# Performance work log

Measured on AMD Instinct MI355X. Metric: run time of the kernel, lower is better.

Reference implementation:

```python
import jax, jax.numpy as jnp
import numpy as np
import math

NUM_USER, NUM_COURSE, NUM_TEACHER, NUM_SCHOOL = 100000, 10000, 5000, 3000
D = 16
B, LS, LT, LSC = 1024, 200, 10, 5
NC, LU, LS2, LT2 = 100, 50, 3, 5


def setup_inputs() -> dict:
    key = jax.random.key(0)
    ks = jax.random.split(key, 32)
    sig = 1.0 / D  # torch init: normal(0, 1/num_dim) on ALL params (overwrites padding row too)
    p = lambda k, shp: jax.random.normal(k, shp, jnp.float32) * sig
    ri = lambda k, shp, hi: jax.random.randint(k, shp, 0, hi)
    inp = {}
    inp['user_idx']       = ri(ks[0], (B, 1), NUM_USER)
    inp['user_sequence']  = ri(ks[1], (B, LS), NUM_COURSE + 1)   # may hit padding idx
    inp['user_teachers']  = ri(ks[2], (B, LT), NUM_TEACHER + 1)
    inp['user_school']    = ri(ks[3], (B, LSC), NUM_SCHOOL + 1)
    inp['user_len_seq']     = jax.random.randint(ks[4], (B, 1), 1, LS + 1).astype(jnp.float32)
    inp['user_len_teacher'] = jax.random.randint(ks[5], (B, 1), 1, LT + 1).astype(jnp.float32)
    inp['user_len_school']  = jax.random.randint(ks[6], (B, 1), 1, LSC + 1).astype(jnp.float32)
    inp['course_set']     = ri(ks[7], (B, NC), NUM_COURSE)
    inp['course_user']    = ri(ks[8], (B, NC, LU), NUM_USER + 1)
    inp['course_school']  = ri(ks[9], (B, NC, LS2), NUM_SCHOOL + 1)
    inp['course_teacher'] = ri(ks[10], (B, NC, LT2), NUM_TEACHER + 1)
    inp['course_len_u']       = jax.random.randint(ks[11], (B, NC), 1, LU + 1).astype(jnp.float32)
    inp['course_len_teacher'] = jax.random.randint(ks[12], (B, NC), 1, LT2 + 1).astype(jnp.float32)
    # learned parameters (jax layout: Linear weight is [in, out])
    inp['user_table']    = p(ks[13], (NUM_USER + 1, D))
    inp['course_table']  = p(ks[14], (NUM_COURSE + 1, D))
    inp['teacher_table'] = p(ks[15], (NUM_TEACHER + 1, D))
    inp['school_table']  = p(ks[16], (NUM_SCHOOL + 1, D))
    inp['Qw'] = p(ks[17], (D, D)); inp['Qb'] = p(ks[18], (D,))
    inp['Kw'] = p(ks[19], (D, D)); inp['Kb'] = p(ks[20], (D,))
    inp['g1w'] = p(ks[21], (2 * D, D)); inp['g1b'] = p(ks[22], (D,))
    inp['g2w'] = p(ks[23], (D, D));     inp['g2b'] = p(ks[24], (D,))
    inp['caw1'] = p(ks[25], (D, D)); inp['cab1'] = p(ks[26], (D,))
    inp['caw2'] = p(ks[27], (D, 1))
    return inp


def _transformer(x, Qw, Qb, Kw, Kb):
    # x: [B, L, d] -> [B, d]. Faithful to source: K is RESHAPED (not transposed) to [B, d, L].
    b, L, d = x.shape
    Q = jax.nn.relu(x @ Qw + Qb)                       # [B, L, d]
    K = jax.nn.relu(x @ Kw + Kb).reshape(b, d, L)      # reshape, as in source
    s = jnp.matmul(Q, K) / math.sqrt(d)                # [B, L, L]
    s = jnp.where(jnp.eye(L, dtype=bool), jnp.float32(1e-32), s)  # diag set to 1e-32
    su = jax.nn.softmax(s, axis=2)
    a = jnp.matmul(su, x)                              # [B, L, d]
    return a.mean(axis=1)


def reference(user_idx, user_sequence, user_teachers, user_school,
              user_len_seq, user_len_teacher, user_len_school,
              course_set, course_user, course_school, course_teacher,
              course_len_u, course_len_teacher,
              user_table, course_table, teacher_table, school_table,
              Qw, Qb, Kw, Kb, g1w, g1b, g2w, g2b, caw1, cab1, caw2):
    # ---- user side ----
    user_emb = user_table[user_idx[:, 0]]                       # [B, d]
    seq_emb = course_table[user_sequence]                       # [B, LS, d]
    seq_rep = _transformer(seq_emb, Qw, Qb, Kw, Kb)             # [B, d]
    ut_mean = teacher_table[user_teachers].sum(axis=1) / user_len_teacher
    us_mean = school_table[user_school].sum(axis=1) / user_len_school
    agg = (seq_rep + ut_mean + us_mean) / 3.0
    h = jnp.concatenate([user_emb, agg], axis=1)                # [B, 2d]
    user_final = jax.nn.relu(h @ g1w + g1b) @ g2w + g2b         # [B, d]
    # ---- course side ----
    course_emb = course_table[course_set]                       # [B, Nc, d]
    cu_mean = user_table[course_user].sum(axis=2) / course_len_u[..., None]
    cs_sum  = school_table[course_school].sum(axis=2)           # note: no division (as in source)
    ct_mean = teacher_table[course_teacher].sum(axis=2) / course_len_teacher[..., None]
    nb = jnp.stack([cu_mean, cs_sum, ct_mean], axis=2)          # [B, Nc, 3, d]
    att = jax.nn.softmax(jax.nn.sigmoid(nb @ caw1 + cab1) @ caw2, axis=2)
    _course_agg = (nb * att).sum(axis=2)  # computed in source but unused (dead code)
    # ---- score ----
    out = jnp.sum(user_final[:, None, :] * course_emb, axis=2)  # [B, Nc]
    return out
```

## Files before the change

### kernel.cpp

```cpp
#include <hip/hip_runtime.h>
#include <hip/hip_bf16.h>

#define NBATCH 1024
#define LSEQ   200
#define DD     16
#define LTT    10
#define LSCH   5
#define NCC    100

#define XT_S   232
#define KT_S   24

#define QSCALE 0.3606737602f

typedef __bf16 bf16_4 __attribute__((ext_vector_type(4)));
typedef float  f32x4  __attribute__((ext_vector_type(4)));
typedef short  short4v __attribute__((ext_vector_type(4)));
typedef unsigned int uint2v __attribute__((ext_vector_type(2)));

__device__ __forceinline__ int kswz(int j) { return ((j >> 3) ^ (j >> 6)) & 1; }

__device__ __forceinline__ f32x4 mfma16(bf16_4 a, bf16_4 b, f32x4 c) {
#if __has_builtin(__builtin_amdgcn_mfma_f32_16x16x16bf16_1k)
    return __builtin_amdgcn_mfma_f32_16x16x16bf16_1k(
        __builtin_bit_cast(short4v, a), __builtin_bit_cast(short4v, b), c, 0, 0, 0);
#else
    uint2v au = __builtin_bit_cast(uint2v, a);
    uint2v bu = __builtin_bit_cast(uint2v, b);
    asm("v_mfma_f32_16x16x16_bf16 %0, %1, %2, %0" : "+v"(c) : "v"(au), "v"(bu));
    return c;
#endif
}

__global__ __launch_bounds__(256, 4) void hin_kernel(
    const int*   __restrict__ user_idx,
    const int*   __restrict__ user_sequence,
    const int*   __restrict__ user_teachers,
    const int*   __restrict__ user_school,
    const float* __restrict__ user_len_teacher,
    const float* __restrict__ user_len_school,
    const int*   __restrict__ course_set,
    const float* __restrict__ user_table,
    const float* __restrict__ course_table,
    const float* __restrict__ teacher_table,
    const float* __restrict__ school_table,
    const float* __restrict__ Qw, const float* __restrict__ Qb,
    const float* __restrict__ Kw, const float* __restrict__ Kb,
    const float* __restrict__ g1w, const float* __restrict__ g1b,
    const float* __restrict__ g2w, const float* __restrict__ g2b,
    float*       __restrict__ out)
{
    __shared__ __align__(16) __bf16 xt[DD * XT_S];
    __shared__ __align__(16) __bf16 kt[208 * KT_S];
    __shared__ float red[4][DD];
    __shared__ __align__(16) float tot12t[64];
    __shared__ float uf[DD];
    __shared__ float gst[800];
    __shared__ float rows_pre[256];
    __shared__ float lens[2];

    const int b    = blockIdx.x;
    const int t    = threadIdx.x;
    const int w    = t >> 6;
    const int lane = t & 63;
    const int grp  = lane >> 4;
    const int li   = lane & 15;

    if (t < 128)
        xt[(t >> 3)*XT_S + 200 + (t & 7)] = (__bf16)0.f;
    else {
        const int i = t - 128;
        kt[(200 + (i >> 4))*KT_S + (i & 15)] = (__bf16)0.f;
    }
    for (int i = t; i < 800; i += 256) {
        float v;
        if      (i < 512) v = g1w[i];
        else if (i < 528) v = g1b[i - 512];
        else if (i < 784) v = g2w[i - 528];
        else              v = g2b[i - 784];
        gst[i] = v;
    }
    if (t < 16)       rows_pre[t] = user_table[user_idx[b]*DD + t];
    else if (t < 176) { const int i = t - 16;
        rows_pre[t] = teacher_table[user_teachers[b*LTT + (i >> 4)]*DD + (i & 15)]; }
    else if (t < 256) { const int i = t - 176;
        rows_pre[t] = school_table[user_school[b*LSCH + (i >> 4)]*DD + (i & 15)]; }
    if (t == 0) { lens[0] = user_len_teacher[b]; lens[1] = user_len_school[b]; }

    const int wu = __builtin_amdgcn_readfirstlane(w);
    const int dr = li - grp*4;

    bf16_4 qf0, qf1, qf2, qf12;
    {
        bf16_4 wq, wk;
        #pragma unroll
        for (int e = 0; e < 4; e++) {
            wq[e] = (__bf16)(Qw[(grp*4 + e)*DD + li] * QSCALE);
            wk[e] = (__bf16)(Kw[(grp*4 + e)*DD + li]);
        }
        const float4 qb4 = *(const float4*)&Qb[grp*4];
        float qbias[4] = {qb4.x*QSCALE, qb4.y*QSCALE, qb4.z*QSCALE, qb4.w*QSCALE};
        const float kbias = Kb[li];

        auto compute_qk = [&](int l0, bf16_4& qout, bool do_scatter) {
            const int lrow = l0 + li;
            const int idx = (lrow < LSEQ) ? user_sequence[b*LSEQ + lrow] : 0;
            const float4 xv = *(const float4*)&course_table[idx*DD + grp*4];
            bf16_4 xf;
            xf[0] = (__bf16)xv.x; xf[1] = (__bf16)xv.y;
            xf[2] = (__bf16)xv.z; xf[3] = (__bf16)xv.w;
            if (do_scatter && lrow < LSEQ) {
                #pragma unroll
                for (int e = 0; e < 4; e++)
                    xt[(grp*4 + e)*XT_S + lrow] = xf[e];
            }
            const f32x4 zc = {0.f, 0.f, 0.f, 0.f};
            f32x4 qv = mfma16(wq, xf, zc);
            f32x4 kv = mfma16(xf, wk, zc);
            #pragma unroll
            for (int r = 0; r < 4; r++)
                qout[r] = (__bf16)fmaxf(qv[r] + qbias[r], 0.f);
            if (do_scatter) {
                #pragma unroll
                for (int r = 0; r < 4; r++) {
                    const int krow = l0 + grp*4 + r;
                    if (krow < LSEQ) {
                        const float val = fmaxf(kv[r] + kbias, 0.f);
                        const int f = krow*DD + li;
                        const int p = f / 200;
                        const int j = f - p*200;
                        kt[j*KT_S + (p ^ (kswz(j) << 3))] = (__bf16)val;
                    }
                }
            }
        };
        compute_qk(wu*16,       qf0, true);
        compute_qk((wu+4)*16,   qf1, true);
        compute_qk((wu+8)*16,   qf2, true);
        compute_qk(192,         qf12, wu == 0);
    }
    __syncthreads();

    bf16_4 onesb;
    #pragma unroll
    for (int i = 0; i < 4; i++) onesb[i] = (__bf16)1.0f;

    const int mt0 = wu, mt1 = wu + 4, mt2 = wu + 8;
    const int jlo = (wu == 0) ? 0 : (3*wu + 1);
    const int jhi = 3*wu + 4;

    f32x4 ao0 = {0.f,0.f,0.f,0.f}, aD0 = {0.f,0.f,0.f,0.f};
    f32x4 ao1 = {0.f,0.f,0.f,0.f}, aD1 = {0.f,0.f,0.f,0.f};
    f32x4 ao2 = {0.f,0.f,0.f,0.f}, aD2 = {0.f,0.f,0.f,0.f};
    f32x4 ao3 = {0.f,0.f,0.f,0.f}, aD3 = {0.f,0.f,0.f,0.f};

    #pragma unroll
    for (int jt = 0; jt < 13; jt++) {
        const int jr = jt*16 + li;
        const bf16_4 kf = *(const bf16_4*)&kt[jr*KT_S + ((grp*4) ^ (kswz(jr) << 3))];
        const bf16_4 xb = *(const bf16_4*)&xt[li*XT_S + jt*16 + grp*4];
        const f32x4 zc = {0.f, 0.f, 0.f, 0.f};
        f32x4 s0 = mfma16(kf, qf0, zc);
        f32x4 s1 = mfma16(kf, qf1, zc);
        f32x4 s2 = mfma16(kf, qf2, zc);
        bf16_4 p0, p1, p2;
        #pragma unroll
        for (int r = 0; r < 4; r++) {
            float v0 = __builtin_amdgcn_exp2f(s0[r]);
            float v1 = __builtin_amdgcn_exp2f(s1[r]);
            float v2 = __builtin_amdgcn_exp2f(s2[r]);
            if (jt == 12 && grp >= 2) { v0 = 0.f; v1 = 0.f; v2 = 0.f; }
            if (jt == mt0 && dr == r) v0 = 1.0f;
            if (jt == mt1 && dr == r) v1 = 1.0f;
            if (jt == mt2 && dr == r) v2 = 1.0f;
            p0[r] = (__bf16)v0; p1[r] = (__bf16)v1; p2[r] = (__bf16)v2;
        }
        aD0 = mfma16(p0, onesb, aD0);  ao0 = mfma16(p0, xb, ao0);
        aD1 = mfma16(p1, onesb, aD1);  ao1 = mfma16(p1, xb, ao1);
        aD2 = mfma16(p2, onesb, aD2);  ao2 = mfma16(p2, xb, ao2);
        if (jt >= jlo && jt < jhi) {
            f32x4 s3 = mfma16(kf, qf12, zc);
            bf16_4 p3;
            #pragma unroll
            for (int r = 0; r < 4; r++) {
                float v3 = __builtin_amdgcn_exp2f(s3[r]);
                if (jt == 12 && grp >= 2) v3 = 0.f;
                if (jt == 12 && dr == r)  v3 = 1.0f;
                p3[r] = (__bf16)v3;
            }
            aD3 = mfma16(p3, onesb, aD3);  ao3 = mfma16(p3, xb, ao3);
        }
    }

    float wsum = 0.f;
    #pragma unroll
    for (int r = 0; r < 4; r++) {
        wsum += ao0[r] * __builtin_amdgcn_rcpf(aD0[r]);
        wsum += ao1[r] * __builtin_amdgcn_rcpf(aD1[r]);
        wsum += ao2[r] * __builtin_amdgcn_rcpf(aD2[r]);
    }
    if (li == 0) {
        #pragma unroll
        for (int r = 0; r < 4; r++)
            tot12t[(grp*4 + r)*4 + w] = aD3[r];
    }
    __syncthreads();

    #pragma unroll
    for (int r = 0; r < 4; r++) {
        const int q = grp*4 + r;
        const float4 p4 = *(const float4*)&tot12t[q*4];
        const float dsum = (p4.x + p4.y) + (p4.z + p4.w);
        if (192 + q < LSEQ)
            wsum += ao3[r] * __builtin_amdgcn_rcpf(dsum);
    }

    wsum += __shfl_xor(wsum, 16);
    wsum += __shfl_xor(wsum, 32);
    if (lane < DD) red[w][lane] = wsum;
    __syncthreads();

    float4 ce0, ce1, ce2, ce3;
    if (t < NCC) {
        const int ci = course_set[b*NCC + t];
        const float* ce = &course_table[ci*DD];
        ce0 = *(const float4*)&ce[0];
        ce1 = *(const float4*)&ce[4];
        ce2 = *(const float4*)&ce[8];
        ce3 = *(const float4*)&ce[12];
    }

    if (w == 0) {
        const float ue  = rows_pre[li];
        const float seq = (red[0][li] + red[1][li] + red[2][li] + red[3][li]) * (1.0f / LSEQ);
        float uts = 0.f;
        #pragma unroll
        for (int i = 0; i < LTT; i++)  uts += rows_pre[16 + i*16 + li];
        float uss = 0.f;
        #pragma unroll
        for (int i = 0; i < LSCH; i++) uss += rows_pre[176 + i*16 + li];
        const float agg = (seq + uts / lens[0] + uss / lens[1]) * (1.0f / 3.0f);
        float a1 = gst[512 + li];
        #pragma unroll
        for (int k = 0; k < 16; k++) a1 = fmaf(__shfl(ue,  k), gst[k*DD + li], a1);
        #pragma unroll
        for (int k = 0; k < 16; k++) a1 = fmaf(__shfl(agg, k), gst[(16 + k)*DD + li], a1);
        const float hidv = fmaxf(a1, 0.f);
        float a2 = gst[784 + li];
        #pragma unroll
        for (int k = 0; k < 16; k++) a2 = fmaf(__shfl(hidv, k), gst[528 + k*DD + li], a2);
        if (lane < DD) uf[lane] = a2;
    }
    __syncthreads();

    if (t < NCC) {
        const float4 u0 = *(const float4*)&uf[0];
        const float4 u1 = *(const float4*)&uf[4];
        const float4 u2 = *(const float4*)&uf[8];
        const float4 u3 = *(const float4*)&uf[12];
        float s = ce0.x*u0.x + ce0.y*u0.y + ce0.z*u0.z + ce0.w*u0.w;
        s      += ce1.x*u1.x + ce1.y*u1.y + ce1.z*u1.z + ce1.w*u1.w;
        s      += ce2.x*u2.x + ce2.y*u2.y + ce2.z*u2.z + ce2.w*u2.w;
        s      += ce3.x*u3.x + ce3.y*u3.y + ce3.z*u3.z + ce3.w*u3.w;
        out[b*NCC + t] = s;
    }
}

extern "C" void kernel_launch(void* const* d_in, const int* in_sizes, int n_in,
                              void* d_out, int out_size, void* d_ws, size_t ws_size,
                              hipStream_t stream) {
    const int*   user_idx         = (const int*)  d_in[0];
    const int*   user_sequence    = (const int*)  d_in[1];
    const int*   user_teachers    = (const int*)  d_in[2];
    const int*   user_school      = (const int*)  d_in[3];
    const float* user_len_teacher = (const float*)d_in[5];
    const float* user_len_school  = (const float*)d_in[6];
    const int*   course_set       = (const int*)  d_in[7];
    const float* user_table       = (const float*)d_in[13];
    const float* course_table     = (const float*)d_in[14];
    const float* teacher_table    = (const float*)d_in[15];
    const float* school_table     = (const float*)d_in[16];
    const float* Qw  = (const float*)d_in[17];
    const float* Qb  = (const float*)d_in[18];
    const float* Kw  = (const float*)d_in[19];
    const float* Kb  = (const float*)d_in[20];
    const float* g1w = (const float*)d_in[21];
    const float* g1b = (const float*)d_in[22];
    const float* g2w = (const float*)d_in[23];
    const float* g2b = (const float*)d_in[24];

    float* outp = (float*)d_out;

    hipLaunchKernelGGL(hin_kernel, dim3(NBATCH), dim3(256), 0, stream,
                       user_idx, user_sequence, user_teachers, user_school,
                       user_len_teacher, user_len_school, course_set,
                       user_table, course_table, teacher_table, school_table,
                       Qw, Qb, Kw, Kb, g1w, g1b, g2w, g2b, outp);
}
```

Measured before the change: 20.24 us.

## Split attention across two blocks per batch and move the MLP tail into a second kernel

The single fused kernel becomes two kernels. The attention kernel launches two blocks per batch row, each handling half of the query tiles with at most two tiles per wave, and writes its partial sums to workspace. A small tail kernel then gathers the user, teacher and school embeddings, runs the MLP and computes the course scores. The aim is more parallelism and occupancy (launch bounds raised to 8) with lower register pressure. In exchange, both blocks recompute the full Q/K projection and LDS staging, and the split adds a second launch plus a global-memory round trip.

```diff
diff --git a/kernel.cpp b/kernel.cpp
--- a/kernel.cpp
+++ b/kernel.cpp
@@ -32,34 +32,20 @@
 #endif
 }
 
-__global__ __launch_bounds__(256, 4) void hin_kernel(
-    const int*   __restrict__ user_idx,
+__global__ __launch_bounds__(256, 8) void hin_attn(
     const int*   __restrict__ user_sequence,
-    const int*   __restrict__ user_teachers,
-    const int*   __restrict__ user_school,
-    const float* __restrict__ user_len_teacher,
-    const float* __restrict__ user_len_school,
-    const int*   __restrict__ course_set,
-    const float* __restrict__ user_table,
     const float* __restrict__ course_table,
-    const float* __restrict__ teacher_table,
-    const float* __restrict__ school_table,
     const float* __restrict__ Qw, const float* __restrict__ Qb,
     const float* __restrict__ Kw, const float* __restrict__ Kb,
-    const float* __restrict__ g1w, const float* __restrict__ g1b,
-    const float* __restrict__ g2w, const float* __restrict__ g2b,
-    float*       __restrict__ out)
+    float*       __restrict__ ws)
 {
     __shared__ __align__(16) __bf16 xt[DD * XT_S];
     __shared__ __align__(16) __bf16 kt[208 * KT_S];
     __shared__ float red[4][DD];
-    __shared__ __align__(16) float tot12t[64];
-    __shared__ float uf[DD];
-    __shared__ float gst[800];
-    __shared__ float rows_pre[256];
-    __shared__ float lens[2];
-
-    const int b    = blockIdx.x;
+
+    const int bid  = blockIdx.x;
+    const int b    = bid >> 1;
+    const int q    = bid & 1;
     const int t    = threadIdx.x;
     const int w    = t >> 6;
     const int lane = t & 63;
@@ -72,20 +58,6 @@
         const int i = t - 128;
         kt[(200 + (i >> 4))*KT_S + (i & 15)] = (__bf16)0.f;
     }
-    for (int i = t; i < 800; i += 256) {
-        float v;
-        if      (i < 512) v = g1w[i];
-        else if (i < 528) v = g1b[i - 512];
-        else if (i < 784) v = g2w[i - 528];
-        else              v = g2b[i - 784];
-        gst[i] = v;
-    }
-    if (t < 16)       rows_pre[t] = user_table[user_idx[b]*DD + t];
-    else if (t < 176) { const int i = t - 16;
-        rows_pre[t] = teacher_table[user_teachers[b*LTT + (i >> 4)]*DD + (i & 15)]; }
-    else if (t < 256) { const int i = t - 176;
-        rows_pre[t] = school_table[user_school[b*LSCH + (i >> 4)]*DD + (i & 15)]; }
-    if (t == 0) { lens[0] = user_len_teacher[b]; lens[1] = user_len_school[b]; }
 
     const int wu = __builtin_amdgcn_readfirstlane(w);
     const int dr = li - grp*4;
@@ -134,91 +106,83 @@
                 }
             }
         };
-        compute_qk(wu*16,       qf0, true);
-        compute_qk((wu+4)*16,   qf1, true);
-        compute_qk((wu+8)*16,   qf2, true);
-        compute_qk(192,         qf12, wu == 0);
+        compute_qk(wu*16,     qf0, true);
+        compute_qk((wu+4)*16, qf1, true);
+        compute_qk((wu+8)*16, qf2, true);
+        compute_qk(192,       qf12, wu == 0);
     }
     __syncthreads();
+
+    int tA, tB; bool hasB; bf16_4 qfA, qfB;
+    if (q == 0)       { tA = wu;     qfA = qf0; tB = wu + 4; qfB = qf1;  hasB = (wu != 3); }
+    else if (wu == 0) { tA = 8;      qfA = qf2; tB = 12;     qfB = qf12; hasB = true; }
+    else if (wu == 3) { tA = 7;      qfA = qf1; tB = 11;     qfB = qf2;  hasB = true; }
+    else              { tA = 8 + wu; qfA = qf2; tB = 0;      qfB = qf0;  hasB = false; }
 
     bf16_4 onesb;
     #pragma unroll
     for (int i = 0; i < 4; i++) onesb[i] = (__bf16)1.0f;
 
-    const int mt0 = wu, mt1 = wu + 4, mt2 = wu + 8;
-    const int jlo = (wu == 0) ? 0 : (3*wu + 1);
-    const int jhi = 3*wu + 4;
-
-    f32x4 ao0 = {0.f,0.f,0.f,0.f}, aD0 = {0.f,0.f,0.f,0.f};
-    f32x4 ao1 = {0.f,0.f,0.f,0.f}, aD1 = {0.f,0.f,0.f,0.f};
-    f32x4 ao2 = {0.f,0.f,0.f,0.f}, aD2 = {0.f,0.f,0.f,0.f};
-    f32x4 ao3 = {0.f,0.f,0.f,0.f}, aD3 = {0.f,0.f,0.f,0.f};
-
-    #pragma unroll
-    for (int jt = 0; jt < 13; jt++) {
-        const int jr = jt*16 + li;
-        const bf16_4 kf = *(const bf16_4*)&kt[jr*KT_S + ((grp*4) ^ (kswz(jr) << 3))];
-        const bf16_4 xb = *(const bf16_4*)&xt[li*XT_S + jt*16 + grp*4];
-        const f32x4 zc = {0.f, 0.f, 0.f, 0.f};
-        f32x4 s0 = mfma16(kf, qf0, zc);
-        f32x4 s1 = mfma16(kf, qf1, zc);
-        f32x4 s2 = mfma16(kf, qf2, zc);
-        bf16_4 p0, p1, p2;
-        #pragma unroll
-        for (int r = 0; r < 4; r++) {
-            float v0 = __builtin_amdgcn_exp2f(s0[r]);
-            float v1 = __builtin_amdgcn_exp2f(s1[r]);
-            float v2 = __builtin_amdgcn_exp2f(s2[r]);
-            if (jt == 12 && grp >= 2) { v0 = 0.f; v1 = 0.f; v2 = 0.f; }
-            if (jt == mt0 && dr == r) v0 = 1.0f;
-            if (jt == mt1 && dr == r) v1 = 1.0f;
-            if (jt == mt2 && dr == r) v2 = 1.0f;
-            p0[r] = (__bf16)v0; p1[r] = (__bf16)v1; p2[r] = (__bf16)v2;
-        }
-        aD0 = mfma16(p0, onesb, aD0);  ao0 = mfma16(p0, xb, ao0);
-        aD1 = mfma16(p1, onesb, aD1);  ao1 = mfma16(p1, xb, ao1);
-        aD2 = mfma16(p2, onesb, aD2);  ao2 = mfma16(p2, xb, ao2);
-        if (jt >= jlo && jt < jhi) {
-            f32x4 s3 = mfma16(kf, qf12, zc);
-            bf16_4 p3;
+    float wsum = 0.f;
+    auto attend = [&](int mt, bf16_4 qf) {
+        f32x4 ao = {0.f,0.f,0.f,0.f}, aD = {0.f,0.f,0.f,0.f};
+        #pragma unroll
+        for (int jt = 0; jt < 13; jt++) {
+            const int jr = jt*16 + li;
+            const bf16_4 kf = *(const bf16_4*)&kt[jr*KT_S + ((grp*4) ^ (kswz(jr) << 3))];
+            const bf16_4 xb = *(const bf16_4*)&xt[li*XT_S + jt*16 + grp*4];
+            const f32x4 zc = {0.f, 0.f, 0.f, 0.f};
+            f32x4 s = mfma16(kf, qf, zc);
+            bf16_4 p;
             #pragma unroll
             for (int r = 0; r < 4; r++) {
-                float v3 = __builtin_amdgcn_exp2f(s3[r]);
-                if (jt == 12 && grp >= 2) v3 = 0.f;
-                if (jt == 12 && dr == r)  v3 = 1.0f;
-                p3[r] = (__bf16)v3;
+                float v = __builtin_amdgcn_exp2f(s[r]);
+                if (jt == 12 && grp >= 2) v = 0.f;
+                if (jt == mt && dr == r)  v = 1.0f;
+                p[r] = (__bf16)v;
             }
-            aD3 = mfma16(p3, onesb, aD3);  ao3 = mfma16(p3, xb, ao3);
+            aD = mfma16(p, onesb, aD);
+            ao = mfma16(p, xb, ao);
         }
-    }
-
-    float wsum = 0.f;
-    #pragma unroll
-    for (int r = 0; r < 4; r++) {
-        wsum += ao0[r] * __builtin_amdgcn_rcpf(aD0[r]);
-        wsum += ao1[r] * __builtin_amdgcn_rcpf(aD1[r]);
-        wsum += ao2[r] * __builtin_amdgcn_rcpf(aD2[r]);
-    }
-    if (li == 0) {
-        #pragma unroll
-        for (int r = 0; r < 4; r++)
-            tot12t[(grp*4 + r)*4 + w] = aD3[r];
-    }
-    __syncthreads();
-
-    #pragma unroll
-    for (int r = 0; r < 4; r++) {
-        const int q = grp*4 + r;
-        const float4 p4 = *(const float4*)&tot12t[q*4];
-        const float dsum = (p4.x + p4.y) + (p4.z + p4.w);
-        if (192 + q < LSEQ)
-            wsum += ao3[r] * __builtin_amdgcn_rcpf(dsum);
-    }
+        #pragma unroll
+        for (int r = 0; r < 4; r++) {
+            const int grow = mt*16 + grp*4 + r;
+            if (grow < LSEQ)
+                wsum += ao[r] * __builtin_amdgcn_rcpf(aD[r]);
+        }
+    };
+    attend(tA, qfA);
+    if (hasB) attend(tB, qfB);
 
     wsum += __shfl_xor(wsum, 16);
     wsum += __shfl_xor(wsum, 32);
     if (lane < DD) red[w][lane] = wsum;
     __syncthreads();
+
+    if (t < DD)
+        ws[(b*2 + q)*DD + t] = (red[0][t] + red[1][t]) + (red[2][t] + red[3][t]);
+}
+
+__global__ __launch_bounds__(128) void hin_tail(
+    const int*   __restrict__ user_idx,
+    const int*   __restrict__ user_teachers,
+    const int*   __restrict__ user_school,
+    const float* __restrict__ user_len_teacher,
+    const float* __restrict__ user_len_school,
+    const int*   __restrict__ course_set,
+    const float* __restrict__ user_table,
+    const float* __restrict__ course_table,
+    const float* __restrict__ teacher_table,
+    const float* __restrict__ school_table,
+    const float* __restrict__ g1w, const float* __restrict__ g1b,
+    const float* __restrict__ g2w, const float* __restrict__ g2b,
+    const float* __restrict__ ws,
+    float*       __restrict__ out)
+{
+    __shared__ float uf[DD];
+
+    const int b = blockIdx.x;
+    const int t = threadIdx.x;
 
     float4 ce0, ce1, ce2, ce3;
     if (t < NCC) {
@@ -230,26 +194,29 @@
         ce3 = *(const float4*)&ce[12];
     }
 
-    if (w == 0) {
-        const float ue  = rows_pre[li];
-        const float seq = (red[0][li] + red[1][li] + red[2][li] + red[3][li]) * (1.0f / LSEQ);
+    if (t < 64) {
+        const int li = t & 15;
+        const float seq = (ws[b*2*DD + li] + ws[(b*2 + 1)*DD + li]) * (1.0f / LSEQ);
+        const float ue  = user_table[user_idx[b]*DD + li];
         float uts = 0.f;
         #pragma unroll
-        for (int i = 0; i < LTT; i++)  uts += rows_pre[16 + i*16 + li];
+        for (int i = 0; i < LTT; i++)
+            uts += teacher_table[user_teachers[b*LTT + i]*DD + li];
         float uss = 0.f;
         #pragma unroll
-        for (int i = 0; i < LSCH; i++) uss += rows_pre[176 + i*16 + li];
-        const float agg = (seq + uts / lens[0] + uss / lens[1]) * (1.0f / 3.0f);
-        float a1 = gst[512 + li];
-        #pragma unroll
-        for (int k = 0; k < 16; k++) a1 = fmaf(__shfl(ue,  k), gst[k*DD + li], a1);
-        #pragma unroll
-        for (int k = 0; k < 16; k++) a1 = fmaf(__shfl(agg, k), gst[(16 + k)*DD + li], a1);
+        for (int i = 0; i < LSCH; i++)
+            uss += school_table[user_school[b*LSCH + i]*DD + li];
+        const float agg = (seq + uts / user_len_teacher[b] + uss / user_len_school[b]) * (1.0f / 3.0f);
+        float a1 = g1b[li];
+        #pragma unroll
+        for (int k = 0; k < 16; k++) a1 = fmaf(__shfl(ue,  k), g1w[k*DD + li], a1);
+        #pragma unroll
+        for (int k = 0; k < 16; k++) a1 = fmaf(__shfl(agg, k), g1w[(16 + k)*DD + li], a1);
         const float hidv = fmaxf(a1, 0.f);
-        float a2 = gst[784 + li];
-        #pragma unroll
-        for (int k = 0; k < 16; k++) a2 = fmaf(__shfl(hidv, k), gst[528 + k*DD + li], a2);
-        if (lane < DD) uf[lane] = a2;
+        float a2 = g2b[li];
+        #pragma unroll
+        for (int k = 0; k < 16; k++) a2 = fmaf(__shfl(hidv, k), g2w[k*DD + li], a2);
+        if (t < DD) uf[t] = a2;
     }
     __syncthreads();
 
@@ -290,10 +257,13 @@
     const float* g2b = (const float*)d_in[24];
 
     float* outp = (float*)d_out;
-
-    hipLaunchKernelGGL(hin_kernel, dim3(NBATCH), dim3(256), 0, stream,
-                       user_idx, user_sequence, user_teachers, user_school,
+    float* ws   = (float*)d_ws;
+
+    hipLaunchKernelGGL(hin_attn, dim3(NBATCH*2), dim3(256), 0, stream,
+                       user_sequence, course_table, Qw, Qb, Kw, Kb, ws);
+    hipLaunchKernelGGL(hin_tail, dim3(NBATCH), dim3(128), 0, stream,
+                       user_idx, user_teachers, user_school,
                        user_len_teacher, user_len_school, course_set,
                        user_table, course_table, teacher_table, school_table,
-                       Qw, Qb, Kw, Kb, g1w, g1b, g2w, g2b, outp);
-}
+                       g1w, g1b, g2w, g2b, ws, outp);
+}
```

Result: slower. 28.96 us (+43.1%).

## Double block to 512 threads and give each wave whole query tiles

Applied to the files above, without the earlier changes.

The kernel now launches 512 threads (8 waves) per batch row instead of 256. Each wave computes Q/K for one or two 16-row tiles and attends over them, instead of three tiles plus a slice of a shared 13th tile. This removes the cross-wave partial-denominator exchange and its extra __syncthreads, and shortens each block's serial chain of MFMA and exp work. In exchange, the launch bound of (512, 8) tightens register limits and may cause spills, and load across waves is uneven because only five of the eight waves take a second tile.

```diff
diff --git a/kernel.cpp b/kernel.cpp
--- a/kernel.cpp
+++ b/kernel.cpp
@@ -32,7 +32,7 @@
 #endif
 }
 
-__global__ __launch_bounds__(256, 4) void hin_kernel(
+__global__ __launch_bounds__(512, 8) void hin_kernel(
     const int*   __restrict__ user_idx,
     const int*   __restrict__ user_sequence,
     const int*   __restrict__ user_teachers,
@@ -52,8 +52,7 @@
 {
     __shared__ __align__(16) __bf16 xt[DD * XT_S];
     __shared__ __align__(16) __bf16 kt[208 * KT_S];
-    __shared__ float red[4][DD];
-    __shared__ __align__(16) float tot12t[64];
+    __shared__ float red[8][DD];
     __shared__ float uf[DD];
     __shared__ float gst[800];
     __shared__ float rows_pre[256];
@@ -68,11 +67,11 @@
 
     if (t < 128)
         xt[(t >> 3)*XT_S + 200 + (t & 7)] = (__bf16)0.f;
-    else {
+    else if (t < 320) {
         const int i = t - 128;
-        kt[(200 + (i >> 4))*KT_S + (i & 15)] = (__bf16)0.f;
-    }
-    for (int i = t; i < 800; i += 256) {
+        kt[(200 + (i >> 4) - ((i >> 4) & ~7))*KT_S + 0] = kt[(200 + (i/24))*KT_S + (i % 24)] = (__bf16)0.f;
+    }
+    for (int i = t; i < 800; i += 512) {
         float v;
         if      (i < 512) v = g1w[i];
         else if (i < 528) v = g1b[i - 512];
@@ -90,7 +89,7 @@
     const int wu = __builtin_amdgcn_readfirstlane(w);
     const int dr = li - grp*4;
 
-    bf16_4 qf0, qf1, qf2, qf12;
+    bf16_4 qfA, qfB;
     {
         bf16_4 wq, wk;
         #pragma unroll
@@ -102,14 +101,14 @@
         float qbias[4] = {qb4.x*QSCALE, qb4.y*QSCALE, qb4.z*QSCALE, qb4.w*QSCALE};
         const float kbias = Kb[li];
 
-        auto compute_qk = [&](int l0, bf16_4& qout, bool do_scatter) {
+        auto compute_qk = [&](int l0, bf16_4& qout) {
             const int lrow = l0 + li;
             const int idx = (lrow < LSEQ) ? user_sequence[b*LSEQ + lrow] : 0;
             const float4 xv = *(const float4*)&course_table[idx*DD + grp*4];
             bf16_4 xf;
             xf[0] = (__bf16)xv.x; xf[1] = (__bf16)xv.y;
             xf[2] = (__bf16)xv.z; xf[3] = (__bf16)xv.w;
-            if (do_scatter && lrow < LSEQ) {
+            if (lrow < LSEQ) {
                 #pragma unroll
                 for (int e = 0; e < 4; e++)
                     xt[(grp*4 + e)*XT_S + lrow] = xf[e];
@@ -120,24 +119,20 @@
             #pragma unroll
             for (int r = 0; r < 4; r++)
                 qout[r] = (__bf16)fmaxf(qv[r] + qbias[r], 0.f);
-            if (do_scatter) {
-                #pragma unroll
-                for (int r = 0; r < 4; r++) {
-                    const int krow = l0 + grp*4 + r;
-                    if (krow < LSEQ) {
-                        const float val = fmaxf(kv[r] + kbias, 0.f);
-                        const int f = krow*DD + li;
-                        const int p = f / 200;
-                        const int j = f - p*200;
-                        kt[j*KT_S + (p ^ (kswz(j) << 3))] = (__bf16)val;
-                    }
+            #pragma unroll
+            for (int r = 0; r < 4; r++) {
+                const int krow = l0 + grp*4 + r;
+                if (krow < LSEQ) {
+                    const float val = fmaxf(kv[r] + kbias, 0.f);
+                    const int f = krow*DD + li;
+                    const int p = f / 200;
+                    const int j = f - p*200;
+                    kt[j*KT_S + (p ^ (kswz(j) << 3))] = (__bf16)val;
                 }
             }
         };
-        compute_qk(wu*16,       qf0, true);
-        compute_qk((wu+4)*16,   qf1, true);
-        compute_qk((wu+8)*16,   qf2, true);
-        compute_qk(192,         qf12, wu == 0);
+        compute_qk(wu*16, qfA);
+        if (wu < 5) compute_qk((wu + 8)*16, qfB);
     }
     __syncthreads();
 
@@ -145,75 +140,36 @@
     #pragma unroll
     for (int i = 0; i < 4; i++) onesb[i] = (__bf16)1.0f;
 
-    const int mt0 = wu, mt1 = wu + 4, mt2 = wu + 8;
-    const int jlo = (wu == 0) ? 0 : (3*wu + 1);
-    const int jhi = 3*wu + 4;
-
-    f32x4 ao0 = {0.f,0.f,0.f,0.f}, aD0 = {0.f,0.f,0.f,0.f};
-    f32x4 ao1 = {0.f,0.f,0.f,0.f}, aD1 = {0.f,0.f,0.f,0.f};
-    f32x4 ao2 = {0.f,0.f,0.f,0.f}, aD2 = {0.f,0.f,0.f,0.f};
-    f32x4 ao3 = {0.f,0.f,0.f,0.f}, aD3 = {0.f,0.f,0.f,0.f};
-
-    #pragma unroll
-    for (int jt = 0; jt < 13; jt++) {
-        const int jr = jt*16 + li;
-        const bf16_4 kf = *(const bf16_4*)&kt[jr*KT_S + ((grp*4) ^ (kswz(jr) << 3))];
-        const bf16_4 xb = *(const bf16_4*)&xt[li*XT_S + jt*16 + grp*4];
-        const f32x4 zc = {0.f, 0.f, 0.f, 0.f};
-        f32x4 s0 = mfma16(kf, qf0, zc);
-        f32x4 s1 = mfma16(kf, qf1, zc);
-        f32x4 s2 = mfma16(kf, qf2, zc);
-        bf16_4 p0, p1, p2;
-        #pragma unroll
-        for (int r = 0; r < 4; r++) {
-            float v0 = __builtin_amdgcn_exp2f(s0[r]);
-            float v1 = __builtin_amdgcn_exp2f(s1[r]);
-            float v2 = __builtin_amdgcn_exp2f(s2[r]);
-            if (jt == 12 && grp >= 2) { v0 = 0.f; v1 = 0.f; v2 = 0.f; }
-            if (jt == mt0 && dr == r) v0 = 1.0f;
-            if (jt == mt1 && dr == r) v1 = 1.0f;
-            if (jt == mt2 && dr == r) v2 = 1.0f;
-            p0[r] = (__bf16)v0; p1[r] = (__bf16)v1; p2[r] = (__bf16)v2;
-        }
-        aD0 = mfma16(p0, onesb, aD0);  ao0 = mfma16(p0, xb, ao0);
-        aD1 = mfma16(p1, onesb, aD1);  ao1 = mfma16(p1, xb, ao1);
-        aD2 = mfma16(p2, onesb, aD2);  ao2 = mfma16(p2, xb, ao2);
-        if (jt >= jlo && jt < jhi) {
-            f32x4 s3 = mfma16(kf, qf12, zc);
-            bf16_4 p3;
+    float wsum = 0.f;
+    auto attend = [&](int mt, bf16_4 qf) {
+        f32x4 ao = {0.f,0.f,0.f,0.f}, aD = {0.f,0.f,0.f,0.f};
+        #pragma unroll
+        for (int jt = 0; jt < 13; jt++) {
+            const int jr = jt*16 + li;
+            const bf16_4 kf = *(const bf16_4*)&kt[jr*KT_S + ((grp*4) ^ (kswz(jr) << 3))];
+            const bf16_4 xb = *(const bf16_4*)&xt[li*XT_S + jt*16 + grp*4];
+            const f32x4 zc = {0.f, 0.f, 0.f, 0.f};
+            f32x4 s = mfma16(kf, qf, zc);
+            bf16_4 p;
             #pragma unroll
             for (int r = 0; r < 4; r++) {
-                float v3 = __builtin_amdgcn_exp2f(s3[r]);
-                if (jt == 12 && grp >= 2) v3 = 0.f;
-                if (jt == 12 && dr == r)  v3 = 1.0f;
-                p3[r] = (__bf16)v3;
+                float v = __builtin_amdgcn_exp2f(s[r]);
+                if (jt == 12 && grp >= 2) v = 0.f;
+                if (jt == mt && dr == r)  v = 1.0f;
+                p[r] = (__bf16)v;
             }
-            aD3 = mfma16(p3, onesb, aD3);  ao3 = mfma16(p3, xb, ao3);
+            aD = mfma16(p, onesb, aD);
+            ao = mfma16(p, xb, ao);
         }
-    }
-
-    float wsum = 0.f;
-    #pragma unroll
-    for (int r = 0; r < 4; r++) {
-        wsum += ao0[r] * __builtin_amdgcn_rcpf(aD0[r]);
-        wsum += ao1[r] * __builtin_amdgcn_rcpf(aD1[r]);
-        wsum += ao2[r] * __builtin_amdgcn_rcpf(aD2[r]);
-    }
-    if (li == 0) {
-        #pragma unroll
-        for (int r = 0; r < 4; r++)
-            tot12t[(grp*4 + r)*4 + w] = aD3[r];
-    }
-    __syncthreads();
-
-    #pragma unroll
-    for (int r = 0; r < 4; r++) {
-        const int q = grp*4 + r;
-        const float4 p4 = *(const float4*)&tot12t[q*4];
-        const float dsum = (p4.x + p4.y) + (p4.z + p4.w);
-        if (192 + q < LSEQ)
-            wsum += ao3[r] * __builtin_amdgcn_rcpf(dsum);
-    }
+        #pragma unroll
+        for (int r = 0; r < 4; r++) {
+            const int grow = mt*16 + grp*4 + r;
+            if (grow < LSEQ)
+                wsum += ao[r] * __builtin_amdgcn_rcpf(aD[r]);
+        }
+    };
+    attend(wu, qfA);
+    if (wu < 5) attend(wu + 8, qfB);
 
     wsum += __shfl_xor(wsum, 16);
     wsum += __shfl_xor(wsum, 32);
@@ -232,7 +188,10 @@
 
     if (w == 0) {
         const float ue  = rows_pre[li];
-        const float seq = (red[0][li] + red[1][li] + red[2][li] + red[3][li]) * (1.0f / LSEQ);
+        float seq = 0.f;
+        #pragma unroll
+        for (int i = 0; i < 8; i++) seq += red[i][li];
+        seq *= (1.0f / LSEQ);
         float uts = 0.f;
         #pragma unroll
         for (int i = 0; i < LTT; i++)  uts += rows_pre[16 + i*16 + li];
@@ -291,7 +250,7 @@
 
     float* outp = (float*)d_out;
 
-    hipLaunchKernelGGL(hin_kernel, dim3(NBATCH), dim3(256), 0, stream,
+    hipLaunchKernelGGL(hin_kernel, dim3(NBATCH), dim3(512), 0, stream,
                        user_idx, user_sequence, user_teachers, user_school,
                        user_len_teacher, user_len_school, course_set,
                        user_table, course_table, teacher_table, school_table,
```

Result: slower. 22.31 us (+10.2%).
